# Kernel optimization log

Measured on AMD Instinct MI355X. Metric: run time of the kernel, lower is better.

## Reference

```python
import jax, jax.numpy as jnp
import numpy as np

B, D, E, H, DEPTH, NH, K = 4, 384, 8, 1536, 12, 6, 2
P, NTOK = 16, 197  # patch size, 14*14 patches + cls
EPS = 1e-6


def layernorm(x, w, b):
    m = x.mean(-1, keepdims=True)
    v = ((x - m) ** 2).mean(-1, keepdims=True)
    return (x - m) / jnp.sqrt(v + EPS) * w + b


def attention(x, qkv_w, qkv_b, proj_w, proj_b):
    Bn, N, C = x.shape
    hd = C // NH
    qkv = x @ qkv_w.T + qkv_b                       # [B,N,3C]
    qkv = qkv.reshape(Bn, N, 3, NH, hd).transpose(2, 0, 3, 1, 4)
    q, k, v = qkv[0], qkv[1], qkv[2]                # [B,h,N,hd]
    attn = jax.nn.softmax((q @ k.transpose(0, 1, 3, 2)) * (hd ** -0.5), axis=-1)
    out = (attn @ v).transpose(0, 2, 1, 3).reshape(Bn, N, C)
    return out @ proj_w.T + proj_b


def mlp(x, w1, b1, w2, b2):
    h = jax.nn.gelu(x @ w1.T + b1, approximate=False)
    return h @ w2.T + b2


def moe_ffn(x2d, gw, w1, b1, w2, b2):
    # noiseless top-k gating (eval mode of NoisyTopKGating)
    logits = x2d @ gw                                # [T,E]
    T = logits.shape[0]
    top_vals, top_idx = jax.lax.top_k(logits, K + 1)
    gates_k = jax.nn.softmax(top_vals[:, :K], axis=-1)
    gates = jnp.zeros((T, E), x2d.dtype).at[jnp.arange(T)[:, None], top_idx[:, :K]].set(gates_k)
    # dense per-expert FFN, weighted combine (identical math to SparseDispatcher)
    h = jax.nn.gelu(jnp.einsum('td,edh->teh', x2d, w1) + b1, approximate=False)
    out = jnp.einsum('teh,ehd->ted', h, w2) + b2
    return jnp.einsum('te,ted->td', gates, out)


def forward(x, patch_w, patch_b, cls_token, pos_embed,
            ln1_w, ln1_b, qkv_w, qkv_b, proj_w, proj_b, ln2_w, ln2_b,
            fc1_w, fc1_b, fc2_w, fc2_b,
            gate_w, moe_w1, moe_b1, moe_w2, moe_b2, lnf_w, lnf_b):
    # patch embed: conv k=16 s=16
    feat = jax.lax.conv_general_dilated(x, patch_w, (P, P), 'VALID',
                                        dimension_numbers=('NCHW', 'OIHW', 'NCHW'))
    feat = feat + patch_b[None, :, None, None]
    Bn = feat.shape[0]
    tokens = feat.reshape(Bn, D, -1).transpose(0, 2, 1)          # [B,196,D]
    cls = jnp.broadcast_to(cls_token, (Bn, 1, D))
    h = jnp.concatenate([cls, tokens], axis=1) + pos_embed       # [B,197,D]

    for i in range(DEPTH):
        h = h + attention(layernorm(h, ln1_w[i], ln1_b[i]), qkv_w[i], qkv_b[i], proj_w[i], proj_b[i])
        y = layernorm(h, ln2_w[i], ln2_b[i])
        if i % 2 == 1:
            j = i // 2
            y2 = moe_ffn(y.reshape(-1, D), gate_w[j], moe_w1[j], moe_b1[j], moe_w2[j], moe_b2[j])
            h = h + y2.reshape(Bn, NTOK, D)
        else:
            j = i // 2
            h = h + mlp(y, fc1_w[j], fc1_b[j], fc2_w[j], fc2_b[j])
    return layernorm(h, lnf_w, lnf_b)


def setup_inputs() -> dict:
    key = jax.random.key(0)
    ks = jax.random.split(key, 16)
    rn = lambda k, s, sd=0.02: jax.random.normal(k, s, jnp.float32) * sd
    return {
        'x': jax.random.normal(ks[0], (B, 3, 224, 224), jnp.float32),
        'patch_w': rn(ks[1], (D, 3, P, P)), 'patch_b': jnp.zeros((D,), jnp.float32),
        'cls_token': rn(ks[2], (1, 1, D)), 'pos_embed': rn(ks[3], (1, NTOK, D)),
        'ln1_w': jnp.ones((DEPTH, D), jnp.float32), 'ln1_b': jnp.zeros((DEPTH, D), jnp.float32),
        'qkv_w': rn(ks[4], (DEPTH, 3 * D, D)), 'qkv_b': jnp.zeros((DEPTH, 3 * D), jnp.float32),
        'proj_w': rn(ks[5], (DEPTH, D, D)), 'proj_b': jnp.zeros((DEPTH, D), jnp.float32),
        'ln2_w': jnp.ones((DEPTH, D), jnp.float32), 'ln2_b': jnp.zeros((DEPTH, D), jnp.float32),
        'fc1_w': rn(ks[6], (DEPTH // 2, H, D)), 'fc1_b': jnp.zeros((DEPTH // 2, H), jnp.float32),
        'fc2_w': rn(ks[7], (DEPTH // 2, D, H)), 'fc2_b': jnp.zeros((DEPTH // 2, D), jnp.float32),
        'gate_w': rn(ks[8], (DEPTH // 2, D, E)),
        'moe_w1': rn(ks[9], (DEPTH // 2, E, D, H)), 'moe_b1': jnp.zeros((DEPTH // 2, E, H), jnp.float32),
        'moe_w2': rn(ks[10], (DEPTH // 2, E, H, D)), 'moe_b2': jnp.zeros((DEPTH // 2, E, D), jnp.float32),
        'lnf_w': jnp.ones((D,), jnp.float32), 'lnf_b': jnp.zeros((D,), jnp.float32),
    }


def reference(x, patch_w, patch_b, cls_token, pos_embed,
              ln1_w, ln1_b, qkv_w, qkv_b, proj_w, proj_b, ln2_w, ln2_b,
              fc1_w, fc1_b, fc2_w, fc2_b,
              gate_w, moe_w1, moe_b1, moe_w2, moe_b2, lnf_w, lnf_b):
    return forward(x, patch_w, patch_b, cls_token, pos_embed,
                   ln1_w, ln1_b, qkv_w, qkv_b, proj_w, proj_b, ln2_w, ln2_b,
                   fc1_w, fc1_b, fc2_w, fc2_b,
                   gate_w, moe_w1, moe_b1, moe_w2, moe_b2, lnf_w, lnf_b)
```

## Files before the change

kernel.cpp:

```cpp
#include <hip/hip_runtime.h>
#include <math.h>

#define NBATCH 4
#define NTOK 197
#define TT 788
#define DM 384
#define HM 1536
#define NHEAD 6
#define NEXP 8
#define LD2 72

typedef __attribute__((ext_vector_type(8))) short bf16x8;
typedef __attribute__((ext_vector_type(4))) float f32x4;

__device__ __forceinline__ void f2bf2(float x, short& hi, short& lo) {
    unsigned u = __float_as_uint(x);
    unsigned uh = u + (0x7fffu + ((u >> 16) & 1u));
    hi = (short)(uh >> 16);
    float hf = __uint_as_float(uh & 0xffff0000u);
    float r = x - hf;
    unsigned v = __float_as_uint(r);
    lo = (short)((v + (0x7fffu + ((v >> 16) & 1u))) >> 16);
}
__device__ __forceinline__ float gelu_f(float x) {
    return 0.5f * x * (1.0f + erff(x * 0.7071067811865475f));
}

__global__ void k_ln(const float* __restrict__ X, const float* __restrict__ w,
                     const float* __restrict__ b, float* __restrict__ Y) {
    int t = blockIdx.x, lane = threadIdx.x;
    const float* x = X + (size_t)t * DM;
    float v[6];
    float s = 0.f;
    #pragma unroll
    for (int i = 0; i < 6; ++i) { v[i] = x[lane + i * 64]; s += v[i]; }
    #pragma unroll
    for (int off = 32; off; off >>= 1) s += __shfl_xor(s, off);
    float mean = s * (1.f / 384.f);
    float q = 0.f;
    #pragma unroll
    for (int i = 0; i < 6; ++i) { float d = v[i] - mean; q += d * d; }
    #pragma unroll
    for (int off = 32; off; off >>= 1) q += __shfl_xor(q, off);
    float inv = rsqrtf(q * (1.f / 384.f) + 1e-6f);
    float* y = Y + (size_t)t * DM;
    #pragma unroll
    for (int i = 0; i < 6; ++i) {
        int d = lane + i * 64;
        y[d] = (v[i] - mean) * inv * w[d] + b[d];
    }
}

__global__ __launch_bounds__(256) void k_patch_gemm(
    const float* __restrict__ X, const float* __restrict__ W,
    const float* __restrict__ pb, const float* __restrict__ cls,
    const float* __restrict__ pos, float* __restrict__ H)
{
    const int M = 784, N = 384, K = 768, MT = 13, NT = 6;
    int mt, nt;
    {
        int lane8 = blockIdx.x & 7;
        int idx = blockIdx.x >> 3;
        nt = idx % NT;
        mt = lane8 + 8 * (idx / NT);
        if (mt >= MT) return;
    }
    __shared__ short Ah[64 * LD2], Al[64 * LD2], Bh[64 * LD2], Bl[64 * LD2];
    const int bm = mt * 64, bn = nt * 64;
    const int tid = threadIdx.x;
    const int lane = tid & 63, w = tid >> 6;
    const int wr = w >> 1, wc = w & 1;
    const int r16 = lane & 15, g = lane >> 4;
    const int sr = tid >> 4;
    const int sc = (tid & 15) * 4;
    const float* cvb[4];
    bool aok[4];
    #pragma unroll
    for (int p = 0; p < 4; ++p) {
        int row = bm + sr + p * 16;
        aok[p] = row < M;
        int b = row / 196, pp = row % 196;
        int py = pp / 14, px = pp % 14;
        cvb[p] = X + (size_t)b * 150528 + (size_t)(py * 16) * 224 + px * 16;
    }
    float4 ra[4], rb[4];
    auto LOADT = [&](int k0) {
        int k = k0 + sc;
        int c = k >> 8, ii = (k >> 4) & 15, j = k & 15;
        size_t coff = (size_t)c * 50176 + ii * 224 + j;
        #pragma unroll
        for (int p = 0; p < 4; ++p) {
            ra[p] = aok[p] ? *(const float4*)(cvb[p] + coff) : make_float4(0.f, 0.f, 0.f, 0.f);
            rb[p] = *(const float4*)(W + (size_t)(bn + sr + p * 16) * K + k0 + sc);
        }
    };
    auto STORET = [&]() {
        #pragma unroll
        for (int p = 0; p < 4; ++p) {
            int r = sr + p * 16;
            float4 a4 = ra[p], b4 = rb[p];
            short4 ah, al, bh, bl;
            f2bf2(a4.x, ah.x, al.x); f2bf2(a4.y, ah.y, al.y);
            f2bf2(a4.z, ah.z, al.z); f2bf2(a4.w, ah.w, al.w);
            f2bf2(b4.x, bh.x, bl.x); f2bf2(b4.y, bh.y, bl.y);
            f2bf2(b4.z, bh.z, bl.z); f2bf2(b4.w, bh.w, bl.w);
            *(short4*)&Ah[r * LD2 + sc] = ah; *(short4*)&Al[r * LD2 + sc] = al;
            *(short4*)&Bh[r * LD2 + sc] = bh; *(short4*)&Bl[r * LD2 + sc] = bl;
        }
    };
    f32x4 acc[2][2] = {};
    auto COMPUTE = [&]() {
        #pragma unroll
        for (int kk = 0; kk < 2; ++kk) {
            bf16x8 afh[2], afl[2], bfh[2], bfl[2];
            #pragma unroll
            for (int i = 0; i < 2; ++i) {
                int off = (wr * 32 + i * 16 + r16) * LD2 + kk * 32 + g * 8;
                afh[i] = *(const bf16x8*)&Ah[off];
                afl[i] = *(const bf16x8*)&Al[off];
            }
            #pragma unroll
            for (int j = 0; j < 2; ++j) {
                int off = (wc * 32 + j * 16 + r16) * LD2 + kk * 32 + g * 8;
                bfh[j] = *(const bf16x8*)&Bh[off];
                bfl[j] = *(const bf16x8*)&Bl[off];
            }
            #pragma unroll
            for (int i = 0; i < 2; ++i)
                #pragma unroll
                for (int j = 0; j < 2; ++j) {
                    acc[i][j] = __builtin_amdgcn_mfma_f32_16x16x32_bf16(afl[i], bfh[j], acc[i][j], 0, 0, 0);
                    acc[i][j] = __builtin_amdgcn_mfma_f32_16x16x32_bf16(afh[i], bfl[j], acc[i][j], 0, 0, 0);
                    acc[i][j] = __builtin_amdgcn_mfma_f32_16x16x32_bf16(afh[i], bfh[j], acc[i][j], 0, 0, 0);
                }
        }
    };
    LOADT(0);
    STORET();
    __syncthreads();
    for (int k0 = 64; k0 < K; k0 += 64) {
        LOADT(k0);
        COMPUTE();
        __syncthreads();
        STORET();
        __syncthreads();
    }
    COMPUTE();
    #pragma unroll
    for (int i = 0; i < 2; ++i) {
        #pragma unroll
        for (int j = 0; j < 2; ++j) {
            int n = bn + wc * 32 + j * 16 + r16;
            int mbase = bm + wr * 32 + i * 16 + g * 4;
            #pragma unroll
            for (int r = 0; r < 4; ++r) {
                int m = mbase + r;
                if (m < M) {
                    int b = m / 196, pp = m % 196;
                    int t = b * NTOK + 1 + pp;
                    H[(size_t)t * DM + n] = acc[i][j][r] + pb[n] + pos[(size_t)(1 + pp) * DM + n];
                }
            }
        }
    }
    if (blockIdx.x == 0) {
        for (int idx = tid; idx < NBATCH * DM; idx += 256) {
            int b = idx / DM, d = idx % DM;
            H[(size_t)(b * NTOK) * DM + d] = cls[d] + pos[d];
        }
    }
}

__global__ __launch_bounds__(256) void k_gemm_mfma(
    const float* __restrict__ A, const float* __restrict__ W,
    const float* __restrict__ bias, float* __restrict__ C,
    int M, int N, int K, int flags, int MT, int NT, int wprot, int ksplit,
    const float* __restrict__ lnw, const float* __restrict__ lnb)
{
    int mt, nt, ks = 0;
    {
        int lane8 = blockIdx.x & 7;
        int idx = blockIdx.x >> 3;
        if (ksplit > 1) { ks = idx % ksplit; idx /= ksplit; }
        if (wprot) {
            mt = idx % MT;
            nt = lane8 + 8 * (idx / MT);
            if (nt >= NT) return;
        } else {
            nt = idx % NT;
            mt = lane8 + 8 * (idx / NT);
            if (mt >= MT) return;
        }
    }
    const int Ks = K / ksplit;
    const float* Ab = A + (size_t)ks * Ks;
    const float* Wb = W + (size_t)ks * Ks;
    __shared__ short Ah[64 * LD2], Al[64 * LD2], Bh[64 * LD2], Bl[64 * LD2];
    const int bm = mt * 64, bn = nt * 64;
    const int tid = threadIdx.x;
    const int lane = tid & 63, w = tid >> 6;
    const int wr = w >> 1, wc = w & 1;
    const int r16 = lane & 15, g = lane >> 4;
    const int sr = tid >> 4;
    const int sc = (tid & 15) * 4;
    const bool doln = (flags & 8) != 0;
    float am[4], ai[4];
    #pragma unroll
    for (int p = 0; p < 4; ++p) { am[p] = 0.f; ai[p] = 1.f; }
    if (doln) {
        int j = tid & 15;
        #pragma unroll
        for (int p = 0; p < 4; ++p) {
            int r = bm + sr + p * 16;
            if (r < M) {
                const float* xr = A + (size_t)r * K;
                float s = 0.f, ss = 0.f;
                #pragma unroll
                for (int i = 0; i < 6; ++i) {
                    float4 v = *(const float4*)(xr + j * 4 + i * 64);
                    s += v.x + v.y + v.z + v.w;
                    ss += v.x * v.x + v.y * v.y + v.z * v.z + v.w * v.w;
                }
                #pragma unroll
                for (int off = 1; off < 16; off <<= 1) {
                    s += __shfl_xor(s, off);
                    ss += __shfl_xor(ss, off);
                }
                float mean = s * (1.f / 384.f);
                float var = ss * (1.f / 384.f) - mean * mean;
                am[p] = mean;
                ai[p] = rsqrtf(var + 1e-6f);
            }
        }
    }
    float4 ra[4], rb[4], lw4, lb4;
    auto LOADT = [&](int k0) {
        if (doln) {
            lw4 = *(const float4*)(lnw + k0 + sc);
            lb4 = *(const float4*)(lnb + k0 + sc);
        }
        #pragma unroll
        for (int p = 0; p < 4; ++p) {
            int r = sr + p * 16;
            ra[p] = make_float4(0.f, 0.f, 0.f, 0.f);
            if (bm + r < M) ra[p] = *(const float4*)(Ab + (size_t)(bm + r) * K + k0 + sc);
            rb[p] = *(const float4*)(Wb + (size_t)(bn + r) * K + k0 + sc);
        }
    };
    auto STORET = [&]() {
        #pragma unroll
        for (int p = 0; p < 4; ++p) {
            int r = sr + p * 16;
            float4 a4 = ra[p];
            if (doln) {
                a4.x = (a4.x - am[p]) * ai[p] * lw4.x + lb4.x;
                a4.y = (a4.y - am[p]) * ai[p] * lw4.y + lb4.y;
                a4.z = (a4.z - am[p]) * ai[p] * lw4.z + lb4.z;
                a4.w = (a4.w - am[p]) * ai[p] * lw4.w + lb4.w;
            }
            float4 b4 = rb[p];
            short4 ah, al, bh, bl;
            f2bf2(a4.x, ah.x, al.x); f2bf2(a4.y, ah.y, al.y);
            f2bf2(a4.z, ah.z, al.z); f2bf2(a4.w, ah.w, al.w);
            f2bf2(b4.x, bh.x, bl.x); f2bf2(b4.y, bh.y, bl.y);
            f2bf2(b4.z, bh.z, bl.z); f2bf2(b4.w, bh.w, bl.w);
            *(short4*)&Ah[r * LD2 + sc] = ah; *(short4*)&Al[r * LD2 + sc] = al;
            *(short4*)&Bh[r * LD2 + sc] = bh; *(short4*)&Bl[r * LD2 + sc] = bl;
        }
    };
    f32x4 acc[2][2] = {};
    auto COMPUTE = [&]() {
        #pragma unroll
        for (int kk = 0; kk < 2; ++kk) {
            bf16x8 afh[2], afl[2], bfh[2], bfl[2];
            #pragma unroll
            for (int i = 0; i < 2; ++i) {
                int off = (wr * 32 + i * 16 + r16) * LD2 + kk * 32 + g * 8;
                afh[i] = *(const bf16x8*)&Ah[off];
                afl[i] = *(const bf16x8*)&Al[off];
            }
            #pragma unroll
            for (int j = 0; j < 2; ++j) {
                int off = (wc * 32 + j * 16 + r16) * LD2 + kk * 32 + g * 8;
                bfh[j] = *(const bf16x8*)&Bh[off];
                bfl[j] = *(const bf16x8*)&Bl[off];
            }
            #pragma unroll
            for (int i = 0; i < 2; ++i)
                #pragma unroll
                for (int j = 0; j < 2; ++j) {
                    acc[i][j] = __builtin_amdgcn_mfma_f32_16x16x32_bf16(afl[i], bfh[j], acc[i][j], 0, 0, 0);
                    acc[i][j] = __builtin_amdgcn_mfma_f32_16x16x32_bf16(afh[i], bfl[j], acc[i][j], 0, 0, 0);
                    acc[i][j] = __builtin_amdgcn_mfma_f32_16x16x32_bf16(afh[i], bfh[j], acc[i][j], 0, 0, 0);
                }
        }
    };
    LOADT(0);
    STORET();
    __syncthreads();
    for (int k0 = 64; k0 < Ks; k0 += 64) {
        LOADT(k0);
        COMPUTE();
        __syncthreads();
        STORET();
        __syncthreads();
    }
    COMPUTE();
    #pragma unroll
    for (int i = 0; i < 2; ++i) {
        #pragma unroll
        for (int j = 0; j < 2; ++j) {
            int n = bn + wc * 32 + j * 16 + r16;
            float bb = (bias && ks == 0) ? bias[n] : 0.f;
            int mbase = bm + wr * 32 + i * 16 + g * 4;
            #pragma unroll
            for (int r = 0; r < 4; ++r) {
                int m = mbase + r;
                if (m < M) {
                    float v = acc[i][j][r] + bb;
                    float* cp = C + (size_t)m * N + n;
                    if (flags & 16) {
                        atomicAdd(cp, v);
                    } else {
                        if (flags & 1) v = gelu_f(v);
                        if (flags & 2) v += *cp;
                        *cp = v;
                    }
                }
            }
        }
    }
}

__global__ __launch_bounds__(256) void k_scoresm(const float* __restrict__ QKV,
                                                 float* __restrict__ S) {
    int z = blockIdx.y;
    int b = z / NHEAD, hh = z % NHEAD;
    int i0 = blockIdx.x * 32;
    __shared__ float qs[32][65];
    __shared__ float ks[32][65];
    __shared__ float srow[32][200];
    int tid = threadIdx.x;
    int r = tid >> 3, d0 = (tid & 7) * 8, c0 = (tid & 7) * 4, l8 = tid & 7;
    {
        float4 v0 = make_float4(0,0,0,0), v1 = v0;
        if (i0 + r < NTOK) {
            const float* qp = QKV + ((size_t)(b * NTOK + i0 + r)) * 1152 + hh * 64 + d0;
            v0 = *(const float4*)qp; v1 = *(const float4*)(qp + 4);
        }
        qs[r][d0+0]=v0.x; qs[r][d0+1]=v0.y; qs[r][d0+2]=v0.z; qs[r][d0+3]=v0.w;
        qs[r][d0+4]=v1.x; qs[r][d0+5]=v1.y; qs[r][d0+6]=v1.z; qs[r][d0+7]=v1.w;
    }
    if (l8 == 0) { srow[r][197] = -1e30f; srow[r][198] = -1e30f; srow[r][199] = -1e30f; }
    for (int j0 = 0; j0 < NTOK; j0 += 32) {
        __syncthreads();
        {
            float4 v0 = make_float4(0,0,0,0), v1 = v0;
            if (j0 + r < NTOK) {
                const float* kp = QKV + ((size_t)(b * NTOK + j0 + r)) * 1152 + 384 + hh * 64 + d0;
                v0 = *(const float4*)kp; v1 = *(const float4*)(kp + 4);
            }
            ks[r][d0+0]=v0.x; ks[r][d0+1]=v0.y; ks[r][d0+2]=v0.z; ks[r][d0+3]=v0.w;
            ks[r][d0+4]=v1.x; ks[r][d0+5]=v1.y; ks[r][d0+6]=v1.z; ks[r][d0+7]=v1.w;
        }
        __syncthreads();
        float acc[4] = {0.f, 0.f, 0.f, 0.f};
        #pragma unroll 8
        for (int d = 0; d < 64; ++d) {
            float qv = qs[r][d];
            #pragma unroll
            for (int u = 0; u < 4; ++u) acc[u] += qv * ks[c0 + u][d];
        }
        #pragma unroll
        for (int u = 0; u < 4; ++u) {
            int j = j0 + c0 + u;
            if (j < NTOK) srow[r][j] = acc[u] * 0.125f;
        }
    }
    __syncthreads();
    float m = -1e30f;
    for (int c = l8; c < 200; c += 8) m = fmaxf(m, srow[r][c]);
    #pragma unroll
    for (int off = 1; off < 8; off <<= 1) m = fmaxf(m, __shfl_xor(m, off));
    float s = 0.f;
    for (int c = l8; c < 200; c += 8) {
        float e = expf(srow[r][c] - m);
        srow[r][c] = e;
        s += e;
    }
    #pragma unroll
    for (int off = 1; off < 8; off <<= 1) s += __shfl_xor(s, off);
    float invs = 1.f / s;
    int i = i0 + r;
    if (i < NTOK) {
        float* sp = S + ((size_t)z * NTOK + i) * NTOK;
        for (int c = l8; c < NTOK; c += 8) sp[c] = srow[r][c] * invs;
    }
}

__global__ __launch_bounds__(256) void k_pv(const float* __restrict__ S, const float* __restrict__ QKV,
                                            float* __restrict__ AO) {
    int z = blockIdx.y;
    int b = z / NHEAD, hh = z % NHEAD;
    int i0 = blockIdx.x * 32;
    __shared__ float ps[32][33];
    __shared__ float vs[32][65];
    int tid = threadIdx.x;
    int r = tid >> 3;
    int c4 = (tid & 7) * 4;
    int d0 = (tid & 7) * 8;
    float acc[8] = {};
    for (int k0 = 0; k0 < NTOK; k0 += 32) {
        #pragma unroll
        for (int u = 0; u < 4; ++u) {
            int i = i0 + r, j = k0 + c4 + u;
            ps[r][c4 + u] = (i < NTOK && j < NTOK) ? S[((size_t)z * NTOK + i) * NTOK + j] : 0.f;
        }
        {
            float4 v0 = make_float4(0,0,0,0), v1 = v0;
            if (k0 + r < NTOK) {
                const float* vp = QKV + ((size_t)(b * NTOK + k0 + r)) * 1152 + 768 + hh * 64 + d0;
                v0 = *(const float4*)vp; v1 = *(const float4*)(vp + 4);
            }
            vs[r][d0+0]=v0.x; vs[r][d0+1]=v0.y; vs[r][d0+2]=v0.z; vs[r][d0+3]=v0.w;
            vs[r][d0+4]=v1.x; vs[r][d0+5]=v1.y; vs[r][d0+6]=v1.z; vs[r][d0+7]=v1.w;
        }
        __syncthreads();
        #pragma unroll 8
        for (int kk = 0; kk < 32; ++kk) {
            float pw = ps[r][kk];
            #pragma unroll
            for (int j = 0; j < 8; ++j) acc[j] += pw * vs[kk][d0 + j];
        }
        __syncthreads();
    }
    int i = i0 + r;
    if (i < NTOK) {
        float* op = AO + (size_t)(b * NTOK + i) * DM + hh * 64 + d0;
        #pragma unroll
        for (int j = 0; j < 8; ++j) op[j] = acc[j];
    }
}

__global__ void k_route_ln(const float* __restrict__ H, float* __restrict__ lnstat,
                           const float* __restrict__ lnw, const float* __restrict__ lnb,
                           const float* __restrict__ GW,
                           int* __restrict__ eidx, float* __restrict__ egate) {
    int t = blockIdx.x * 4 + (threadIdx.x >> 6);
    if (t >= TT) return;
    int lane = threadIdx.x & 63;
    const float* x = H + (size_t)t * DM;
    float v[6];
    float s = 0.f, ss = 0.f;
    #pragma unroll
    for (int i = 0; i < 6; ++i) {
        v[i] = x[lane + i * 64];
        s += v[i];
        ss += v[i] * v[i];
    }
    #pragma unroll
    for (int off = 32; off; off >>= 1) { s += __shfl_xor(s, off); ss += __shfl_xor(ss, off); }
    float mean = s * (1.f / 384.f);
    float var = ss * (1.f / 384.f) - mean * mean;
    float inv = rsqrtf(var + 1e-6f);
    if (lane == 0) { lnstat[2 * t] = mean; lnstat[2 * t + 1] = inv; }
    float l8v[NEXP] = {};
    #pragma unroll
    for (int i = 0; i < 6; ++i) {
        int d = lane + i * 64;
        float yv = (v[i] - mean) * inv * lnw[d] + lnb[d];
        const float* g = GW + (size_t)d * NEXP;
        #pragma unroll
        for (int e = 0; e < NEXP; ++e) l8v[e] += yv * g[e];
    }
    #pragma unroll
    for (int e = 0; e < NEXP; ++e) {
        float vv = l8v[e];
        #pragma unroll
        for (int off = 32; off; off >>= 1) vv += __shfl_xor(vv, off);
        l8v[e] = vv;
    }
    if (lane == 0) {
        int b0 = 0;
        #pragma unroll
        for (int e = 1; e < NEXP; ++e) if (l8v[e] > l8v[b0]) b0 = e;
        int b1 = -1;
        #pragma unroll
        for (int e = 0; e < NEXP; ++e) if (e != b0 && (b1 < 0 || l8v[e] > l8v[b1])) b1 = e;
        float e1 = expf(l8v[b1] - l8v[b0]);
        float denom = 1.f + e1;
        eidx[2 * t] = b0; eidx[2 * t + 1] = b1;
        egate[2 * t] = 1.f / denom; egate[2 * t + 1] = e1 / denom;
    }
}

__global__ void k_pscatter(int* __restrict__ cnt, int* __restrict__ basep,
                           const int* __restrict__ eidx, const float* __restrict__ egate,
                           int* __restrict__ slot_tok, float* __restrict__ slot_gate) {
    __shared__ int hist[NEXP];
    __shared__ int bp[NEXP];
    __shared__ int fl[NEXP];
    int tid = threadIdx.x;
    if (tid < NEXP) { hist[tid] = 0; fl[tid] = 0; }
    __syncthreads();
    for (int i = tid; i < 2 * TT; i += 256) atomicAdd(&hist[eidx[i]], 1);
    __syncthreads();
    if (tid == 0) {
        int s = 0;
        for (int e = 0; e < NEXP; ++e) { bp[e] = s; s += hist[e]; }
    }
    __syncthreads();
    if (tid < NEXP) { cnt[tid] = hist[tid]; basep[tid] = bp[tid]; }
    for (int t = tid; t < TT; t += 256) {
        #pragma unroll
        for (int k = 0; k < 2; ++k) {
            int e = eidx[2 * t + k];
            int pos = atomicAdd(&fl[e], 1);
            int s = bp[e] + pos;
            slot_tok[s] = t;
            slot_gate[s] = egate[2 * t + k];
        }
    }
}

__global__ __launch_bounds__(256) void k_moe1_mfma(
    const float* __restrict__ H, const float* __restrict__ lnstat,
    const float* __restrict__ lnw, const float* __restrict__ lnb,
    const float* __restrict__ W1, const float* __restrict__ B1,
    const int* __restrict__ slot_tok, const int* __restrict__ cnt, const int* __restrict__ basep,
    float* __restrict__ HID)
{
    const int e = blockIdx.x & 7;
    const int idx = blockIdx.x >> 3;
    const int mt = idx % 13;
    const int nt = idx / 13;
    const int c = cnt[e];
    const int r0 = mt * 64;
    if (r0 >= c) return;
    const int sbase = basep[e];
    const int n0 = nt * 64;
    const float* W = W1 + (size_t)e * DM * HM;
    const float* B1e = B1 + (size_t)e * HM;
    __shared__ short Ah[64 * LD2], Al[64 * LD2], Bh[64 * LD2], Bl[64 * LD2];
    const int tid = threadIdx.x;
    const int lane = tid & 63, w = tid >> 6;
    const int wr = w >> 1, wc = w & 1;
    const int r16 = lane & 15, g = lane >> 4;
    const int sr = tid >> 4, sc = (tid & 15) * 4;
    const int kq = (tid >> 4) * 4;
    int tokp[4];
    float am4[4], ai4[4];
    #pragma unroll
    for (int p = 0; p < 4; ++p) {
        int m = r0 + sr + p * 16;
        tokp[p] = (m < c) ? slot_tok[sbase + m] : -1;
        am4[p] = 0.f; ai4[p] = 1.f;
        if (tokp[p] >= 0) { am4[p] = lnstat[2 * tokp[p]]; ai4[p] = lnstat[2 * tokp[p] + 1]; }
    }
    f32x4 acc[2][2] = {};
    for (int k0 = 0; k0 < DM; k0 += 64) {
        float4 lw4 = *(const float4*)(lnw + k0 + sc);
        float4 lb4 = *(const float4*)(lnb + k0 + sc);
        #pragma unroll
        for (int p = 0; p < 4; ++p) {
            int r = sr + p * 16;
            float4 a4 = make_float4(0.f, 0.f, 0.f, 0.f);
            if (tokp[p] >= 0) {
                a4 = *(const float4*)(H + (size_t)tokp[p] * DM + k0 + sc);
                a4.x = (a4.x - am4[p]) * ai4[p] * lw4.x + lb4.x;
                a4.y = (a4.y - am4[p]) * ai4[p] * lw4.y + lb4.y;
                a4.z = (a4.z - am4[p]) * ai4[p] * lw4.z + lb4.z;
                a4.w = (a4.w - am4[p]) * ai4[p] * lw4.w + lb4.w;
            }
            short4 ah, al;
            f2bf2(a4.x, ah.x, al.x); f2bf2(a4.y, ah.y, al.y);
            f2bf2(a4.z, ah.z, al.z); f2bf2(a4.w, ah.w, al.w);
            *(short4*)&Ah[r * LD2 + sc] = ah; *(short4*)&Al[r * LD2 + sc] = al;
        }
        {
            float4 b4[4];
            #pragma unroll
            for (int i = 0; i < 4; ++i)
                b4[i] = *(const float4*)(W + (size_t)(k0 + kq + i) * HM + n0 + sc);
            float col[4][4] = {
                { b4[0].x, b4[1].x, b4[2].x, b4[3].x },
                { b4[0].y, b4[1].y, b4[2].y, b4[3].y },
                { b4[0].z, b4[1].z, b4[2].z, b4[3].z },
                { b4[0].w, b4[1].w, b4[2].w, b4[3].w } };
            #pragma unroll
            for (int u = 0; u < 4; ++u) {
                short4 hh, ll;
                f2bf2(col[u][0], hh.x, ll.x); f2bf2(col[u][1], hh.y, ll.y);
                f2bf2(col[u][2], hh.z, ll.z); f2bf2(col[u][3], hh.w, ll.w);
                *(short4*)&Bh[(sc + u) * LD2 + kq] = hh;
                *(short4*)&Bl[(sc + u) * LD2 + kq] = ll;
            }
        }
        __syncthreads();
        #pragma unroll
        for (int kk = 0; kk < 2; ++kk) {
            bf16x8 afh[2], afl[2], bfh[2], bfl[2];
            #pragma unroll
            for (int i = 0; i < 2; ++i) {
                int off = (wr * 32 + i * 16 + r16) * LD2 + kk * 32 + g * 8;
                afh[i] = *(const bf16x8*)&Ah[off];
                afl[i] = *(const bf16x8*)&Al[off];
            }
            #pragma unroll
            for (int j = 0; j < 2; ++j) {
                int off = (wc * 32 + j * 16 + r16) * LD2 + kk * 32 + g * 8;
                bfh[j] = *(const bf16x8*)&Bh[off];
                bfl[j] = *(const bf16x8*)&Bl[off];
            }
            #pragma unroll
            for (int i = 0; i < 2; ++i)
                #pragma unroll
                for (int j = 0; j < 2; ++j) {
                    acc[i][j] = __builtin_amdgcn_mfma_f32_16x16x32_bf16(afl[i], bfh[j], acc[i][j], 0, 0, 0);
                    acc[i][j] = __builtin_amdgcn_mfma_f32_16x16x32_bf16(afh[i], bfl[j], acc[i][j], 0, 0, 0);
                    acc[i][j] = __builtin_amdgcn_mfma_f32_16x16x32_bf16(afh[i], bfh[j], acc[i][j], 0, 0, 0);
                }
        }
        __syncthreads();
    }
    #pragma unroll
    for (int i = 0; i < 2; ++i) {
        #pragma unroll
        for (int j = 0; j < 2; ++j) {
            int n = n0 + wc * 32 + j * 16 + r16;
            float bb = B1e[n];
            #pragma unroll
            for (int r = 0; r < 4; ++r) {
                int m = r0 + wr * 32 + i * 16 + g * 4 + r;
                if (m < c)
                    HID[(size_t)(sbase + m) * HM + n] = gelu_f(acc[i][j][r] + bb);
            }
        }
    }
}

__global__ __launch_bounds__(256) void k_moe2_mfma(
    const float* __restrict__ HID, const float* __restrict__ W2, const float* __restrict__ B2,
    const int* __restrict__ cnt, const int* __restrict__ basep,
    const int* __restrict__ slot_tok, const float* __restrict__ slot_gate,
    float* __restrict__ H)
{
    const int e = blockIdx.x & 7;
    const int idx = blockIdx.x >> 3;
    const int mt = idx % 13;
    const int rest = idx / 13;
    const int nt = rest % 6;
    const int ks = rest / 6;
    const int c = cnt[e];
    const int r0 = mt * 64;
    if (r0 >= c) return;
    const int sbase = basep[e];
    const int n0 = nt * 64;
    const int kbase = ks * 384;
    const float* W = W2 + (size_t)e * HM * DM + (size_t)kbase * DM;
    const float* B2e = B2 + (size_t)e * DM;
    __shared__ short Ah[64 * LD2], Al[64 * LD2], Bh[64 * LD2], Bl[64 * LD2];
    const int tid = threadIdx.x;
    const int lane = tid & 63, w = tid >> 6;
    const int wr = w >> 1, wc = w & 1;
    const int r16 = lane & 15, g = lane >> 4;
    const int sr = tid >> 4, sc = (tid & 15) * 4;
    const int kq = (tid >> 4) * 4;
    f32x4 acc[2][2] = {};
    for (int k0 = 0; k0 < 384; k0 += 64) {
        #pragma unroll
        for (int p = 0; p < 4; ++p) {
            int r = sr + p * 16;
            int m = r0 + r;
            float4 a4 = make_float4(0.f, 0.f, 0.f, 0.f);
            if (m < c) a4 = *(const float4*)(HID + (size_t)(sbase + m) * HM + kbase + k0 + sc);
            short4 ah, al;
            f2bf2(a4.x, ah.x, al.x); f2bf2(a4.y, ah.y, al.y);
            f2bf2(a4.z, ah.z, al.z); f2bf2(a4.w, ah.w, al.w);
            *(short4*)&Ah[r * LD2 + sc] = ah; *(short4*)&Al[r * LD2 + sc] = al;
        }
        {
            float4 b4[4];
            #pragma unroll
            for (int i = 0; i < 4; ++i)
                b4[i] = *(const float4*)(W + (size_t)(k0 + kq + i) * DM + n0 + sc);
            float col[4][4] = {
                { b4[0].x, b4[1].x, b4[2].x, b4[3].x },
                { b4[0].y, b4[1].y, b4[2].y, b4[3].y },
                { b4[0].z, b4[1].z, b4[2].z, b4[3].z },
                { b4[0].w, b4[1].w, b4[2].w, b4[3].w } };
            #pragma unroll
            for (int u = 0; u < 4; ++u) {
                short4 hh, ll;
                f2bf2(col[u][0], hh.x, ll.x); f2bf2(col[u][1], hh.y, ll.y);
                f2bf2(col[u][2], hh.z, ll.z); f2bf2(col[u][3], hh.w, ll.w);
                *(short4*)&Bh[(sc + u) * LD2 + kq] = hh;
                *(short4*)&Bl[(sc + u) * LD2 + kq] = ll;
            }
        }
        __syncthreads();
        #pragma unroll
        for (int kk = 0; kk < 2; ++kk) {
            bf16x8 afh[2], afl[2], bfh[2], bfl[2];
            #pragma unroll
            for (int i = 0; i < 2; ++i) {
                int off = (wr * 32 + i * 16 + r16) * LD2 + kk * 32 + g * 8;
                afh[i] = *(const bf16x8*)&Ah[off];
                afl[i] = *(const bf16x8*)&Al[off];
            }
            #pragma unroll
            for (int j = 0; j < 2; ++j) {
                int off = (wc * 32 + j * 16 + r16) * LD2 + kk * 32 + g * 8;
                bfh[j] = *(const bf16x8*)&Bh[off];
                bfl[j] = *(const bf16x8*)&Bl[off];
            }
            #pragma unroll
            for (int i = 0; i < 2; ++i)
                #pragma unroll
                for (int j = 0; j < 2; ++j) {
                    acc[i][j] = __builtin_amdgcn_mfma_f32_16x16x32_bf16(afl[i], bfh[j], acc[i][j], 0, 0, 0);
                    acc[i][j] = __builtin_amdgcn_mfma_f32_16x16x32_bf16(afh[i], bfl[j], acc[i][j], 0, 0, 0);
                    acc[i][j] = __builtin_amdgcn_mfma_f32_16x16x32_bf16(afh[i], bfh[j], acc[i][j], 0, 0, 0);
                }
        }
        __syncthreads();
    }
    #pragma unroll
    for (int i = 0; i < 2; ++i) {
        #pragma unroll
        for (int j = 0; j < 2; ++j) {
            int n = n0 + wc * 32 + j * 16 + r16;
            float bb = (ks == 0) ? B2e[n] : 0.f;
            #pragma unroll
            for (int r = 0; r < 4; ++r) {
                int m = r0 + wr * 32 + i * 16 + g * 4 + r;
                if (m < c) {
                    int tok = slot_tok[sbase + m];
                    float gt = slot_gate[sbase + m];
                    atomicAdd(&H[(size_t)tok * DM + n], gt * (acc[i][j][r] + bb));
                }
            }
        }
    }
}

extern "C" void kernel_launch(void* const* d_in, const int* in_sizes, int n_in,
                              void* d_out, int out_size, void* d_ws, size_t ws_size,
                              hipStream_t stream) {
    const float* x         = (const float*)d_in[0];
    const float* patch_w   = (const float*)d_in[1];
    const float* patch_b   = (const float*)d_in[2];
    const float* cls_token = (const float*)d_in[3];
    const float* pos_embed = (const float*)d_in[4];
    const float* ln1_w     = (const float*)d_in[5];
    const float* ln1_b     = (const float*)d_in[6];
    const float* qkv_w     = (const float*)d_in[7];
    const float* qkv_b     = (const float*)d_in[8];
    const float* proj_w    = (const float*)d_in[9];
    const float* proj_b    = (const float*)d_in[10];
    const float* ln2_w     = (const float*)d_in[11];
    const float* ln2_b     = (const float*)d_in[12];
    const float* fc1_w     = (const float*)d_in[13];
    const float* fc1_b     = (const float*)d_in[14];
    const float* fc2_w     = (const float*)d_in[15];
    const float* fc2_b     = (const float*)d_in[16];
    const float* gate_w    = (const float*)d_in[17];
    const float* moe_w1    = (const float*)d_in[18];
    const float* moe_b1    = (const float*)d_in[19];
    const float* moe_w2    = (const float*)d_in[20];
    const float* moe_b2    = (const float*)d_in[21];
    const float* lnf_w     = (const float*)d_in[22];
    const float* lnf_b     = (const float*)d_in[23];
    float* out = (float*)d_out;

    float* wsf = (float*)d_ws;
    float* regA     = wsf;
    float* moehid   = regA;
    float* h     = regA + 2420736;
    float* spare = h + 302592;
    float* qkvb  = spare + 302592;
    float* attno = qkvb + 907776;
    float* regC  = attno + 302592;
    float* S    = regC;
    float* hid  = regC;
    float* egate = regC + 1210368;
    int* ib       = (int*)(egate + 1576);
    int* eidx     = ib;
    int* slot_tok = ib + 1576;
    int* slot_of  = ib + 3152;
    int* cnt      = ib + 4728;
    int* basep    = ib + 4736;
    float* lnstat = (float*)(ib + 4752);
    float* slot_gate = lnstat + 1576;

    k_patch_gemm<<<96, 256, 0, stream>>>(x, patch_w, patch_b, cls_token, pos_embed, h);

    for (int l = 0; l < 12; ++l) {
        k_gemm_mfma<<<312, 256, 0, stream>>>(h, qkv_w + (size_t)l * 1152 * DM,
                                             qkv_b + l * 1152, qkvb, TT, 1152, DM, 8,
                                             13, 18, 1, 1,
                                             ln1_w + l * DM, ln1_b + l * DM);
        k_scoresm<<<dim3(7, NBATCH * NHEAD), 256, 0, stream>>>(qkvb, S);
        k_pv<<<dim3(7, NBATCH * NHEAD), 256, 0, stream>>>(S, qkvb, attno);
        k_gemm_mfma<<<192, 256, 0, stream>>>(attno, proj_w + (size_t)l * DM * DM,
                                             proj_b + l * DM, h, TT, DM, DM, 16,
                                             13, 6, 0, 2, nullptr, nullptr);
        int j = l >> 1;
        if ((l & 1) == 0) {
            k_gemm_mfma<<<312, 256, 0, stream>>>(h, fc1_w + (size_t)j * HM * DM,
                                                 fc1_b + j * HM, hid, TT, HM, DM, 9,
                                                 13, 24, 1, 1,
                                                 ln2_w + l * DM, ln2_b + l * DM);
            k_gemm_mfma<<<384, 256, 0, stream>>>(hid, fc2_w + (size_t)j * DM * HM,
                                                 fc2_b + j * DM, h, TT, DM, HM, 16,
                                                 13, 6, 0, 4, nullptr, nullptr);
        } else {
            k_route_ln<<<197, 256, 0, stream>>>(h, lnstat, ln2_w + l * DM, ln2_b + l * DM,
                                                gate_w + (size_t)j * DM * NEXP, eidx, egate);
            k_pscatter<<<1, 256, 0, stream>>>(cnt, basep, eidx, egate, slot_tok, slot_gate);
            k_moe1_mfma<<<8 * 13 * 24, 256, 0, stream>>>(
                h, lnstat, ln2_w + l * DM, ln2_b + l * DM,
                moe_w1 + (size_t)j * NEXP * DM * HM, moe_b1 + (size_t)j * NEXP * HM,
                slot_tok, cnt, basep, moehid);
            k_moe2_mfma<<<8 * 13 * 24, 256, 0, stream>>>(
                moehid, moe_w2 + (size_t)j * NEXP * HM * DM, moe_b2 + (size_t)j * NEXP * DM,
                cnt, basep, slot_tok, slot_gate, h);
        }
    }
    k_ln<<<TT, 64, 0, stream>>>(h, lnf_w, lnf_b, out);
}
```

Baseline: 1.681 ms.

## Split-K QKV/FC1 into two partial buffers and fuse MoE scatter into routing

The QKV and FC1 GEMMs now run split-K with two halves written to separate buffers, doubling the block count. The partial sums are combined where they are consumed: the attention kernels add the two halves, and FC2 sums them and applies GELU as it loads. The separate single-block MoE scatter kernel is removed. Routing now atomically appends tokens into fixed per-expert slot regions, with per-layer counters zeroed once at the start. This trades extra partial-buffer traffic and recomputed GELU per FC2 tile for more parallelism and one fewer serial launch per MoE layer, and the token order within each expert becomes nondeterministic.

```diff
diff --git a/kernel.cpp b/kernel.cpp
--- a/kernel.cpp
+++ b/kernel.cpp
@@ -56,14 +56,14 @@
     const float* __restrict__ pb, const float* __restrict__ cls,
     const float* __restrict__ pos, float* __restrict__ H)
 {
-    const int M = 784, N = 384, K = 768, MT = 13, NT = 6;
+    const int M = 784, N = 384, K = 768, NT = 6;
     int mt, nt;
     {
         int lane8 = blockIdx.x & 7;
         int idx = blockIdx.x >> 3;
         nt = idx % NT;
         mt = lane8 + 8 * (idx / NT);
-        if (mt >= MT) return;
+        if (mt >= 13) return;
     }
     __shared__ short Ah[64 * LD2], Al[64 * LD2], Bh[64 * LD2], Bl[64 * LD2];
     const int bm = mt * 64, bn = nt * 64;
@@ -172,8 +172,9 @@
 }
 
 __global__ __launch_bounds__(256) void k_gemm_mfma(
-    const float* __restrict__ A, const float* __restrict__ W,
-    const float* __restrict__ bias, float* __restrict__ C,
+    const float* __restrict__ A, const float* __restrict__ A2,
+    const float* __restrict__ W, const float* __restrict__ bias,
+    float* __restrict__ C, float* __restrict__ C2,
     int M, int N, int K, int flags, int MT, int NT, int wprot, int ksplit,
     const float* __restrict__ lnw, const float* __restrict__ lnb)
 {
@@ -193,8 +194,11 @@
         }
     }
     const int Ks = K / ksplit;
-    const float* Ab = A + (size_t)ks * Ks;
-    const float* Wb = W + (size_t)ks * Ks;
+    const float* Ab  = A + (size_t)ks * Ks;
+    const float* A2b = A2 ? (A2 + (size_t)ks * Ks) : nullptr;
+    const float* Wb  = W + (size_t)ks * Ks;
+    const float* lnwb = lnw ? (lnw + (size_t)ks * Ks) : nullptr;
+    const float* lnbb = lnb ? (lnb + (size_t)ks * Ks) : nullptr;
     __shared__ short Ah[64 * LD2], Al[64 * LD2], Bh[64 * LD2], Bl[64 * LD2];
     const int bm = mt * 64, bn = nt * 64;
     const int tid = threadIdx.x;
@@ -204,6 +208,7 @@
     const int sr = tid >> 4;
     const int sc = (tid & 15) * 4;
     const bool doln = (flags & 8) != 0;
+    const bool dogelu_a = (flags & 32) != 0;
     float am[4], ai[4];
     #pragma unroll
     for (int p = 0; p < 4; ++p) { am[p] = 0.f; ai[p] = 1.f; }
@@ -233,17 +238,21 @@
             }
         }
     }
-    float4 ra[4], rb[4], lw4, lb4;
+    float4 ra[4], ra2[4], rb[4], lw4, lb4;
     auto LOADT = [&](int k0) {
         if (doln) {
-            lw4 = *(const float4*)(lnw + k0 + sc);
-            lb4 = *(const float4*)(lnb + k0 + sc);
+            lw4 = *(const float4*)(lnwb + k0 + sc);
+            lb4 = *(const float4*)(lnbb + k0 + sc);
         }
         #pragma unroll
         for (int p = 0; p < 4; ++p) {
             int r = sr + p * 16;
             ra[p] = make_float4(0.f, 0.f, 0.f, 0.f);
-            if (bm + r < M) ra[p] = *(const float4*)(Ab + (size_t)(bm + r) * K + k0 + sc);
+            ra2[p] = ra[p];
+            if (bm + r < M) {
+                ra[p] = *(const float4*)(Ab + (size_t)(bm + r) * K + k0 + sc);
+                if (dogelu_a) ra2[p] = *(const float4*)(A2b + (size_t)(bm + r) * K + k0 + sc);
+            }
             rb[p] = *(const float4*)(Wb + (size_t)(bn + r) * K + k0 + sc);
         }
     };
@@ -252,6 +261,12 @@
         for (int p = 0; p < 4; ++p) {
             int r = sr + p * 16;
             float4 a4 = ra[p];
+            if (dogelu_a) {
+                a4.x = gelu_f(a4.x + ra2[p].x);
+                a4.y = gelu_f(a4.y + ra2[p].y);
+                a4.z = gelu_f(a4.z + ra2[p].z);
+                a4.w = gelu_f(a4.w + ra2[p].w);
+            }
             if (doln) {
                 a4.x = (a4.x - am[p]) * ai[p] * lw4.x + lb4.x;
                 a4.y = (a4.y - am[p]) * ai[p] * lw4.y + lb4.y;
@@ -306,6 +321,7 @@
         __syncthreads();
     }
     COMPUTE();
+    float* Cout = (C2 && ks == 1) ? C2 : C;
     #pragma unroll
     for (int i = 0; i < 2; ++i) {
         #pragma unroll
@@ -318,11 +334,12 @@
                 int m = mbase + r;
                 if (m < M) {
                     float v = acc[i][j][r] + bb;
-                    float* cp = C + (size_t)m * N + n;
-                    if (flags & 16) {
+                    float* cp = Cout + (size_t)m * N + n;
+                    if (C2) {
+                        *cp = v;
+                    } else if (flags & 16) {
                         atomicAdd(cp, v);
                     } else {
-                        if (flags & 1) v = gelu_f(v);
                         if (flags & 2) v += *cp;
                         *cp = v;
                     }
@@ -332,7 +349,8 @@
     }
 }
 
-__global__ __launch_bounds__(256) void k_scoresm(const float* __restrict__ QKV,
+__global__ __launch_bounds__(256) void k_scoresm(const float* __restrict__ Q0,
+                                                 const float* __restrict__ Q1,
                                                  float* __restrict__ S) {
     int z = blockIdx.y;
     int b = z / NHEAD, hh = z % NHEAD;
@@ -345,8 +363,11 @@
     {
         float4 v0 = make_float4(0,0,0,0), v1 = v0;
         if (i0 + r < NTOK) {
-            const float* qp = QKV + ((size_t)(b * NTOK + i0 + r)) * 1152 + hh * 64 + d0;
-            v0 = *(const float4*)qp; v1 = *(const float4*)(qp + 4);
+            size_t off = ((size_t)(b * NTOK + i0 + r)) * 1152 + hh * 64 + d0;
+            float4 a0 = *(const float4*)(Q0 + off), b0 = *(const float4*)(Q1 + off);
+            float4 a1 = *(const float4*)(Q0 + off + 4), b1 = *(const float4*)(Q1 + off + 4);
+            v0 = make_float4(a0.x + b0.x, a0.y + b0.y, a0.z + b0.z, a0.w + b0.w);
+            v1 = make_float4(a1.x + b1.x, a1.y + b1.y, a1.z + b1.z, a1.w + b1.w);
         }
         qs[r][d0+0]=v0.x; qs[r][d0+1]=v0.y; qs[r][d0+2]=v0.z; qs[r][d0+3]=v0.w;
         qs[r][d0+4]=v1.x; qs[r][d0+5]=v1.y; qs[r][d0+6]=v1.z; qs[r][d0+7]=v1.w;
@@ -357,8 +378,11 @@
         {
             float4 v0 = make_float4(0,0,0,0), v1 = v0;
             if (j0 + r < NTOK) {
-                const float* kp = QKV + ((size_t)(b * NTOK + j0 + r)) * 1152 + 384 + hh * 64 + d0;
-                v0 = *(const float4*)kp; v1 = *(const float4*)(kp + 4);
+                size_t off = ((size_t)(b * NTOK + j0 + r)) * 1152 + 384 + hh * 64 + d0;
+                float4 a0 = *(const float4*)(Q0 + off), b0 = *(const float4*)(Q1 + off);
+                float4 a1 = *(const float4*)(Q0 + off + 4), b1 = *(const float4*)(Q1 + off + 4);
+                v0 = make_float4(a0.x + b0.x, a0.y + b0.y, a0.z + b0.z, a0.w + b0.w);
+                v1 = make_float4(a1.x + b1.x, a1.y + b1.y, a1.z + b1.z, a1.w + b1.w);
             }
             ks[r][d0+0]=v0.x; ks[r][d0+1]=v0.y; ks[r][d0+2]=v0.z; ks[r][d0+3]=v0.w;
             ks[r][d0+4]=v1.x; ks[r][d0+5]=v1.y; ks[r][d0+6]=v1.z; ks[r][d0+7]=v1.w;
@@ -398,7 +422,9 @@
     }
 }
 
-__global__ __launch_bounds__(256) void k_pv(const float* __restrict__ S, const float* __restrict__ QKV,
+__global__ __launch_bounds__(256) void k_pv(const float* __restrict__ S,
+                                            const float* __restrict__ Q0,
+                                            const float* __restrict__ Q1,
                                             float* __restrict__ AO) {
     int z = blockIdx.y;
     int b = z / NHEAD, hh = z % NHEAD;
@@ -419,8 +445,11 @@
         {
             float4 v0 = make_float4(0,0,0,0), v1 = v0;
             if (k0 + r < NTOK) {
-                const float* vp = QKV + ((size_t)(b * NTOK + k0 + r)) * 1152 + 768 + hh * 64 + d0;
-                v0 = *(const float4*)vp; v1 = *(const float4*)(vp + 4);
+                size_t off = ((size_t)(b * NTOK + k0 + r)) * 1152 + 768 + hh * 64 + d0;
+                float4 a0 = *(const float4*)(Q0 + off), b0 = *(const float4*)(Q1 + off);
+                float4 a1 = *(const float4*)(Q0 + off + 4), b1 = *(const float4*)(Q1 + off + 4);
+                v0 = make_float4(a0.x + b0.x, a0.y + b0.y, a0.z + b0.z, a0.w + b0.w);
+                v1 = make_float4(a1.x + b1.x, a1.y + b1.y, a1.z + b1.z, a1.w + b1.w);
             }
             vs[r][d0+0]=v0.x; vs[r][d0+1]=v0.y; vs[r][d0+2]=v0.z; vs[r][d0+3]=v0.w;
             vs[r][d0+4]=v1.x; vs[r][d0+5]=v1.y; vs[r][d0+6]=v1.z; vs[r][d0+7]=v1.w;
@@ -445,7 +474,8 @@
 __global__ void k_route_ln(const float* __restrict__ H, float* __restrict__ lnstat,
                            const float* __restrict__ lnw, const float* __restrict__ lnb,
                            const float* __restrict__ GW,
-                           int* __restrict__ eidx, float* __restrict__ egate) {
+                           int* __restrict__ slot_tok, float* __restrict__ slot_gate,
+                           int* __restrict__ cntL) {
     int t = blockIdx.x * 4 + (threadIdx.x >> 6);
     if (t >= TT) return;
     int lane = threadIdx.x & 63;
@@ -489,37 +519,13 @@
         for (int e = 0; e < NEXP; ++e) if (e != b0 && (b1 < 0 || l8v[e] > l8v[b1])) b1 = e;
         float e1 = expf(l8v[b1] - l8v[b0]);
         float denom = 1.f + e1;
-        eidx[2 * t] = b0; eidx[2 * t + 1] = b1;
-        egate[2 * t] = 1.f / denom; egate[2 * t + 1] = e1 / denom;
-    }
-}
-
-__global__ void k_pscatter(int* __restrict__ cnt, int* __restrict__ basep,
-                           const int* __restrict__ eidx, const float* __restrict__ egate,
-                           int* __restrict__ slot_tok, float* __restrict__ slot_gate) {
-    __shared__ int hist[NEXP];
-    __shared__ int bp[NEXP];
-    __shared__ int fl[NEXP];
-    int tid = threadIdx.x;
-    if (tid < NEXP) { hist[tid] = 0; fl[tid] = 0; }
-    __syncthreads();
-    for (int i = tid; i < 2 * TT; i += 256) atomicAdd(&hist[eidx[i]], 1);
-    __syncthreads();
-    if (tid == 0) {
-        int s = 0;
-        for (int e = 0; e < NEXP; ++e) { bp[e] = s; s += hist[e]; }
-    }
-    __syncthreads();
-    if (tid < NEXP) { cnt[tid] = hist[tid]; basep[tid] = bp[tid]; }
-    for (int t = tid; t < TT; t += 256) {
-        #pragma unroll
-        for (int k = 0; k < 2; ++k) {
-            int e = eidx[2 * t + k];
-            int pos = atomicAdd(&fl[e], 1);
-            int s = bp[e] + pos;
-            slot_tok[s] = t;
-            slot_gate[s] = egate[2 * t + k];
-        }
+        float g0 = 1.f / denom, g1 = e1 / denom;
+        int p0 = atomicAdd(&cntL[b0], 1);
+        slot_tok[b0 * TT + p0] = t;
+        slot_gate[b0 * TT + p0] = g0;
+        int p1 = atomicAdd(&cntL[b1], 1);
+        slot_tok[b1 * TT + p1] = t;
+        slot_gate[b1 * TT + p1] = g1;
     }
 }
 
@@ -527,17 +533,19 @@
     const float* __restrict__ H, const float* __restrict__ lnstat,
     const float* __restrict__ lnw, const float* __restrict__ lnb,
     const float* __restrict__ W1, const float* __restrict__ B1,
-    const int* __restrict__ slot_tok, const int* __restrict__ cnt, const int* __restrict__ basep,
+    const int* __restrict__ slot_tok, const int* __restrict__ cntL,
     float* __restrict__ HID)
 {
     const int e = blockIdx.x & 7;
     const int idx = blockIdx.x >> 3;
     const int mt = idx % 13;
     const int nt = idx / 13;
-    const int c = cnt[e];
+    const int c = cntL[e];
     const int r0 = mt * 64;
     if (r0 >= c) return;
-    const int sbase = basep[e];
+    int hbase = 0;
+    for (int xx = 0; xx < e; ++xx) hbase += cntL[xx];
+    const int sbase = e * TT;
     const int n0 = nt * 64;
     const float* W = W1 + (size_t)e * DM * HM;
     const float* B1e = B1 + (size_t)e * HM;
@@ -633,7 +641,7 @@
             for (int r = 0; r < 4; ++r) {
                 int m = r0 + wr * 32 + i * 16 + g * 4 + r;
                 if (m < c)
-                    HID[(size_t)(sbase + m) * HM + n] = gelu_f(acc[i][j][r] + bb);
+                    HID[(size_t)(hbase + m) * HM + n] = gelu_f(acc[i][j][r] + bb);
             }
         }
     }
@@ -641,7 +649,7 @@
 
 __global__ __launch_bounds__(256) void k_moe2_mfma(
     const float* __restrict__ HID, const float* __restrict__ W2, const float* __restrict__ B2,
-    const int* __restrict__ cnt, const int* __restrict__ basep,
+    const int* __restrict__ cntL,
     const int* __restrict__ slot_tok, const float* __restrict__ slot_gate,
     float* __restrict__ H)
 {
@@ -651,10 +659,12 @@
     const int rest = idx / 13;
     const int nt = rest % 6;
     const int ks = rest / 6;
-    const int c = cnt[e];
+    const int c = cntL[e];
     const int r0 = mt * 64;
     if (r0 >= c) return;
-    const int sbase = basep[e];
+    int hbase = 0;
+    for (int xx = 0; xx < e; ++xx) hbase += cntL[xx];
+    const int sbase = e * TT;
     const int n0 = nt * 64;
     const int kbase = ks * 384;
     const float* W = W2 + (size_t)e * HM * DM + (size_t)kbase * DM;
@@ -673,7 +683,7 @@
             int r = sr + p * 16;
             int m = r0 + r;
             float4 a4 = make_float4(0.f, 0.f, 0.f, 0.f);
-            if (m < c) a4 = *(const float4*)(HID + (size_t)(sbase + m) * HM + kbase + k0 + sc);
+            if (m < c) a4 = *(const float4*)(HID + (size_t)(hbase + m) * HM + kbase + k0 + sc);
             short4 ah, al;
             f2bf2(a4.x, ah.x, al.x); f2bf2(a4.y, ah.y, al.y);
             f2bf2(a4.z, ah.z, al.z); f2bf2(a4.w, ah.w, al.w);
@@ -774,57 +784,60 @@
     float* out = (float*)d_out;
 
     float* wsf = (float*)d_ws;
-    float* regA     = wsf;
-    float* moehid   = regA;
+    float* regA  = wsf;
     float* h     = regA + 2420736;
     float* spare = h + 302592;
     float* qkvb  = spare + 302592;
     float* attno = qkvb + 907776;
     float* regC  = attno + 302592;
+    float* qkvb1 = regA;
+    float* hid1  = regA;
+    float* moehid = regA;
     float* S    = regC;
-    float* hid  = regC;
-    float* egate = regC + 1210368;
-    int* ib       = (int*)(egate + 1576);
-    int* eidx     = ib;
-    int* slot_tok = ib + 1576;
-    int* slot_of  = ib + 3152;
-    int* cnt      = ib + 4728;
-    int* basep    = ib + 4736;
-    float* lnstat = (float*)(ib + 4752);
-    float* slot_gate = lnstat + 1576;
+    float* hid0 = regC;
+    float* tail = regC + 1210368;
+    float* lnstat    = tail;
+    float* slot_gate = tail + 1576;
+    int*   slot_tok  = (int*)(slot_gate + 6304);
+    int*   cntAll    = slot_tok + 6304;
+
+    hipMemsetAsync(cntAll, 0, 6 * NEXP * sizeof(int), stream);
 
     k_patch_gemm<<<96, 256, 0, stream>>>(x, patch_w, patch_b, cls_token, pos_embed, h);
 
     for (int l = 0; l < 12; ++l) {
-        k_gemm_mfma<<<312, 256, 0, stream>>>(h, qkv_w + (size_t)l * 1152 * DM,
-                                             qkv_b + l * 1152, qkvb, TT, 1152, DM, 8,
-                                             13, 18, 1, 1,
+        k_gemm_mfma<<<624, 256, 0, stream>>>(h, nullptr, qkv_w + (size_t)l * 1152 * DM,
+                                             qkv_b + l * 1152, qkvb, qkvb1,
+                                             TT, 1152, DM, 8, 13, 18, 1, 2,
                                              ln1_w + l * DM, ln1_b + l * DM);
-        k_scoresm<<<dim3(7, NBATCH * NHEAD), 256, 0, stream>>>(qkvb, S);
-        k_pv<<<dim3(7, NBATCH * NHEAD), 256, 0, stream>>>(S, qkvb, attno);
-        k_gemm_mfma<<<192, 256, 0, stream>>>(attno, proj_w + (size_t)l * DM * DM,
-                                             proj_b + l * DM, h, TT, DM, DM, 16,
-                                             13, 6, 0, 2, nullptr, nullptr);
+        k_scoresm<<<dim3(7, NBATCH * NHEAD), 256, 0, stream>>>(qkvb, qkvb1, S);
+        k_pv<<<dim3(7, NBATCH * NHEAD), 256, 0, stream>>>(S, qkvb, qkvb1, attno);
+        k_gemm_mfma<<<192, 256, 0, stream>>>(attno, nullptr, proj_w + (size_t)l * DM * DM,
+                                             proj_b + l * DM, h, nullptr,
+                                             TT, DM, DM, 16, 13, 6, 0, 2,
+                                             nullptr, nullptr);
         int j = l >> 1;
         if ((l & 1) == 0) {
-            k_gemm_mfma<<<312, 256, 0, stream>>>(h, fc1_w + (size_t)j * HM * DM,
-                                                 fc1_b + j * HM, hid, TT, HM, DM, 9,
-                                                 13, 24, 1, 1,
+            k_gemm_mfma<<<624, 256, 0, stream>>>(h, nullptr, fc1_w + (size_t)j * HM * DM,
+                                                 fc1_b + j * HM, hid0, hid1,
+                                                 TT, HM, DM, 8, 13, 24, 1, 2,
                                                  ln2_w + l * DM, ln2_b + l * DM);
-            k_gemm_mfma<<<384, 256, 0, stream>>>(hid, fc2_w + (size_t)j * DM * HM,
-                                                 fc2_b + j * DM, h, TT, DM, HM, 16,
-                                                 13, 6, 0, 4, nullptr, nullptr);
+            k_gemm_mfma<<<384, 256, 0, stream>>>(hid0, hid1, fc2_w + (size_t)j * DM * HM,
+                                                 fc2_b + j * DM, h, nullptr,
+                                                 TT, DM, HM, 16 | 32, 13, 6, 0, 4,
+                                                 nullptr, nullptr);
         } else {
+            int* cntL = cntAll + j * NEXP;
             k_route_ln<<<197, 256, 0, stream>>>(h, lnstat, ln2_w + l * DM, ln2_b + l * DM,
-                                                gate_w + (size_t)j * DM * NEXP, eidx, egate);
-            k_pscatter<<<1, 256, 0, stream>>>(cnt, basep, eidx, egate, slot_tok, slot_gate);
+                                                gate_w + (size_t)j * DM * NEXP,
+                                                slot_tok, slot_gate, cntL);
             k_moe1_mfma<<<8 * 13 * 24, 256, 0, stream>>>(
                 h, lnstat, ln2_w + l * DM, ln2_b + l * DM,
                 moe_w1 + (size_t)j * NEXP * DM * HM, moe_b1 + (size_t)j * NEXP * HM,
-                slot_tok, cnt, basep, moehid);
+                slot_tok, cntL, moehid);
             k_moe2_mfma<<<8 * 13 * 24, 256, 0, stream>>>(
                 moehid, moe_w2 + (size_t)j * NEXP * HM * DM, moe_b2 + (size_t)j * NEXP * DM,
-                cnt, basep, slot_tok, slot_gate, h);
+                cntL, slot_tok, slot_gate, h);
         }
     }
     k_ln<<<TT, 64, 0, stream>>>(h, lnf_w, lnf_b, out);
```

Result: slower. 1.825 ms (+8.6%).

## Split-K the QKV and fc1 GEMMs with atomics, move GELU into fc2 load

Applied to the files above, without the earlier changes.

The QKV and fc1 GEMMs now split K=384 in two and accumulate with atomicAdd into buffers zeroed by hipMemsetAsync, which doubles their block count to 624. Because a split-K epilogue cannot apply GELU, the GELU is moved to the A-tile load of the fc2 GEMM via a new flag. The LayerNorm weight and bias pointers are offset per K split to match. The aim is better CU occupancy. The cost is extra memsets, atomic traffic, and GELU being recomputed once per N-tile in fc2 (six times per element).

```diff
diff --git a/kernel.cpp b/kernel.cpp
--- a/kernel.cpp
+++ b/kernel.cpp
@@ -56,14 +56,14 @@
     const float* __restrict__ pb, const float* __restrict__ cls,
     const float* __restrict__ pos, float* __restrict__ H)
 {
-    const int M = 784, N = 384, K = 768, MT = 13, NT = 6;
+    const int M = 784, N = 384, K = 768, NT = 6;
     int mt, nt;
     {
         int lane8 = blockIdx.x & 7;
         int idx = blockIdx.x >> 3;
         nt = idx % NT;
         mt = lane8 + 8 * (idx / NT);
-        if (mt >= MT) return;
+        if (mt >= 13) return;
     }
     __shared__ short Ah[64 * LD2], Al[64 * LD2], Bh[64 * LD2], Bl[64 * LD2];
     const int bm = mt * 64, bn = nt * 64;
@@ -195,6 +195,8 @@
     const int Ks = K / ksplit;
     const float* Ab = A + (size_t)ks * Ks;
     const float* Wb = W + (size_t)ks * Ks;
+    const float* lnwb = lnw ? (lnw + (size_t)ks * Ks) : nullptr;
+    const float* lnbb = lnb ? (lnb + (size_t)ks * Ks) : nullptr;
     __shared__ short Ah[64 * LD2], Al[64 * LD2], Bh[64 * LD2], Bl[64 * LD2];
     const int bm = mt * 64, bn = nt * 64;
     const int tid = threadIdx.x;
@@ -204,6 +206,7 @@
     const int sr = tid >> 4;
     const int sc = (tid & 15) * 4;
     const bool doln = (flags & 8) != 0;
+    const bool dogelu_a = (flags & 32) != 0;
     float am[4], ai[4];
     #pragma unroll
     for (int p = 0; p < 4; ++p) { am[p] = 0.f; ai[p] = 1.f; }
@@ -236,8 +239,8 @@
     float4 ra[4], rb[4], lw4, lb4;
     auto LOADT = [&](int k0) {
         if (doln) {
-            lw4 = *(const float4*)(lnw + k0 + sc);
-            lb4 = *(const float4*)(lnb + k0 + sc);
+            lw4 = *(const float4*)(lnwb + k0 + sc);
+            lb4 = *(const float4*)(lnbb + k0 + sc);
         }
         #pragma unroll
         for (int p = 0; p < 4; ++p) {
@@ -252,6 +255,12 @@
         for (int p = 0; p < 4; ++p) {
             int r = sr + p * 16;
             float4 a4 = ra[p];
+            if (dogelu_a) {
+                a4.x = gelu_f(a4.x);
+                a4.y = gelu_f(a4.y);
+                a4.z = gelu_f(a4.z);
+                a4.w = gelu_f(a4.w);
+            }
             if (doln) {
                 a4.x = (a4.x - am[p]) * ai[p] * lw4.x + lb4.x;
                 a4.y = (a4.y - am[p]) * ai[p] * lw4.y + lb4.y;
@@ -322,7 +331,6 @@
                     if (flags & 16) {
                         atomicAdd(cp, v);
                     } else {
-                        if (flags & 1) v = gelu_f(v);
                         if (flags & 2) v += *cp;
                         *cp = v;
                     }
@@ -774,20 +782,19 @@
     float* out = (float*)d_out;
 
     float* wsf = (float*)d_ws;
-    float* regA     = wsf;
-    float* moehid   = regA;
+    float* regA  = wsf;
     float* h     = regA + 2420736;
     float* spare = h + 302592;
     float* qkvb  = spare + 302592;
     float* attno = qkvb + 907776;
     float* regC  = attno + 302592;
+    float* moehid = regA;
     float* S    = regC;
     float* hid  = regC;
     float* egate = regC + 1210368;
     int* ib       = (int*)(egate + 1576);
     int* eidx     = ib;
     int* slot_tok = ib + 1576;
-    int* slot_of  = ib + 3152;
     int* cnt      = ib + 4728;
     int* basep    = ib + 4736;
     float* lnstat = (float*)(ib + 4752);
@@ -796,24 +803,28 @@
     k_patch_gemm<<<96, 256, 0, stream>>>(x, patch_w, patch_b, cls_token, pos_embed, h);
 
     for (int l = 0; l < 12; ++l) {
-        k_gemm_mfma<<<312, 256, 0, stream>>>(h, qkv_w + (size_t)l * 1152 * DM,
-                                             qkv_b + l * 1152, qkvb, TT, 1152, DM, 8,
-                                             13, 18, 1, 1,
+        hipMemsetAsync(qkvb, 0, (size_t)TT * 1152 * sizeof(float), stream);
+        k_gemm_mfma<<<624, 256, 0, stream>>>(h, qkv_w + (size_t)l * 1152 * DM,
+                                             qkv_b + l * 1152, qkvb,
+                                             TT, 1152, DM, 8 | 16, 13, 18, 1, 2,
                                              ln1_w + l * DM, ln1_b + l * DM);
         k_scoresm<<<dim3(7, NBATCH * NHEAD), 256, 0, stream>>>(qkvb, S);
         k_pv<<<dim3(7, NBATCH * NHEAD), 256, 0, stream>>>(S, qkvb, attno);
         k_gemm_mfma<<<192, 256, 0, stream>>>(attno, proj_w + (size_t)l * DM * DM,
-                                             proj_b + l * DM, h, TT, DM, DM, 16,
-                                             13, 6, 0, 2, nullptr, nullptr);
+                                             proj_b + l * DM, h,
+                                             TT, DM, DM, 16, 13, 6, 0, 2,
+                                             nullptr, nullptr);
         int j = l >> 1;
         if ((l & 1) == 0) {
-            k_gemm_mfma<<<312, 256, 0, stream>>>(h, fc1_w + (size_t)j * HM * DM,
-                                                 fc1_b + j * HM, hid, TT, HM, DM, 9,
-                                                 13, 24, 1, 1,
+            hipMemsetAsync(hid, 0, (size_t)TT * HM * sizeof(float), stream);
+            k_gemm_mfma<<<624, 256, 0, stream>>>(h, fc1_w + (size_t)j * HM * DM,
+                                                 fc1_b + j * HM, hid,
+                                                 TT, HM, DM, 8 | 16, 13, 24, 1, 2,
                                                  ln2_w + l * DM, ln2_b + l * DM);
             k_gemm_mfma<<<384, 256, 0, stream>>>(hid, fc2_w + (size_t)j * DM * HM,
-                                                 fc2_b + j * DM, h, TT, DM, HM, 16,
-                                                 13, 6, 0, 4, nullptr, nullptr);
+                                                 fc2_b + j * DM, h,
+                                                 TT, DM, HM, 16 | 32, 13, 6, 0, 4,
+                                                 nullptr, nullptr);
         } else {
             k_route_ln<<<197, 256, 0, stream>>>(h, lnstat, ln2_w + l * DM, ln2_b + l * DM,
                                                 gate_w + (size_t)j * DM * NEXP, eidx, egate);
```

Result: slower. 1.748 ms (+4.0%).
